# Kernel optimization log

Measured on AMD Instinct MI355X. Metric: run time of the kernel, lower is better.

Reference implementation:

```python
import jax, jax.numpy as jnp
import numpy as np
import itertools

L, F, T = 16, 2, 2**19          # levels, features/level, hashmap size
BASE, SCALE = 16, 1.5           # base resolution, per-level scale
N = 524288                      # batch of sample points
PRIMES = np.array([1, 2654435761, 805459861, 3674653429], dtype=np.uint32)


def hash_encode(x, table):
    """Multi-resolution hash-grid encoding. x: [N,d] in [0,1); table: [L,T,F]."""
    n, d = x.shape
    corners = jnp.asarray(list(itertools.product([0, 1], repeat=d)), dtype=jnp.uint32)  # [C,d]
    primes = jnp.asarray(PRIMES[:d])
    is_hi = corners.astype(bool)[None]          # [1,C,d]
    outs = []
    for l in range(L):
        res = float(np.floor(BASE * SCALE**l))
        pos = x * res
        p0f = jnp.floor(pos)
        frac = pos - p0f                         # [N,d]
        p0 = p0f.astype(jnp.uint32)
        coords = p0[:, None, :] + corners[None]  # [N,C,d] uint32 (wraps)
        m = coords * primes                      # [N,C,d]
        h = m[..., 0]
        for j in range(1, d):
            h = h ^ m[..., j]
        idx = (h % np.uint32(T)).astype(jnp.int32)              # [N,C]
        w = jnp.where(is_hi, frac[:, None, :], 1.0 - frac[:, None, :]).prod(-1)  # [N,C]
        feat = table[l][idx]                                    # [N,C,F]
        outs.append(jnp.einsum('nc,ncf->nf', w, feat))
    return jnp.concatenate(outs, axis=-1)        # [N, L*F]


def mlp(h, w_in, w_hid, w_out):
    """tcnn-style bias-free MLP, ReLU hidden, linear output."""
    h = jax.nn.relu(h @ w_in)
    for i in range(w_hid.shape[0]):
        h = jax.nn.relu(h @ w_hid[i])
    return h @ w_out


def setup_inputs() -> dict:
    key = jax.random.key(0)
    ks = jax.random.split(key, 20)
    def w(k, shape):
        fan = shape[-2]
        return jax.random.normal(k, shape, jnp.float32) / np.sqrt(fan).astype(np.float32)
    return {
        'x': jax.random.uniform(ks[0], (N, 3), jnp.float32),
        't': jax.random.uniform(ks[1], (1,), jnp.float32),
        'skip_alpha': jax.random.uniform(ks[2], (1,), jnp.float32),
        'table_s': jax.random.normal(ks[3], (L, T, F), jnp.float32) * 1e-2,
        'ws_in': w(ks[4], (32, 64)),
        'ws_hid': w(ks[5], (3, 64, 64)),
        'ws_out': w(ks[6], (64, 64)),
        'table_d': jax.random.normal(ks[7], (L, T, F), jnp.float32) * 1e-2,
        'wd_in': w(ks[8], (32, 64)),
        'wd_hid': w(ks[9], (3, 64, 64)),
        'wd_out': w(ks[10], (64, 64)),
        'w1_in': w(ks[11], (128, 64)),
        'w1_hid': w(ks[12], (1, 64, 64)),
        'w1_out': w(ks[13], (64, 128)),
        'w2_in': w(ks[14], (128, 64)),
        'w2_hid': w(ks[15], (1, 64, 64)),
        'w2_out': w(ks[16], (64, 1)),
    }


def reference(x, t, skip_alpha, table_s, ws_in, ws_hid, ws_out,
              table_d, wd_in, wd_hid, wd_out,
              w1_in, w1_hid, w1_out, w2_in, w2_hid, w2_out):
    static_features = mlp(hash_encode(x, table_s), ws_in, ws_hid, ws_out)          # [N,64]
    t_col = jnp.broadcast_to(t, (x.shape[0], 1))
    x4 = jnp.concatenate([x, t_col], axis=1)                                        # [N,4]
    dynamic_features = mlp(hash_encode(x4, table_d), wd_in, wd_hid, wd_out)        # [N,64]
    features = jnp.concatenate([static_features, dynamic_features], axis=-1)       # [N,128]
    out1 = mlp(features, w1_in, w1_hid, w1_out)                                     # [N,128]
    blended = out1 * skip_alpha + (1.0 - skip_alpha) * features
    return mlp(blended, w2_in, w2_hid, w2_out)                                      # [N,1]
```

## Files before the change

kernel.cpp:

```cpp
#include <hip/hip_runtime.h>
#include <hip/hip_bf16.h>
#include <stdint.h>

#define LVLS 16
#define TSZ  524288
#define TMASK 0x7FFFFu
#define NPTS 524288
#define P1 2654435761u
#define P2 805459861u
#define P3 3674653429u

__constant__ float RES_TAB[16] = {
    16.f, 24.f, 36.f, 54.f, 81.f, 121.f, 182.f, 273.f,
    410.f, 615.f, 922.f, 1383.f, 2075.f, 3113.f, 4670.f, 7006.f};

using f16x8 = __attribute__((ext_vector_type(8))) _Float16;
using f32x4 = __attribute__((ext_vector_type(4))) float;
using u32x8 = __attribute__((ext_vector_type(8))) uint32_t;

union PackF16 { uint32_t u; _Float16 h[2]; };

constexpr int PS = 72;

struct WPtrs { const float* p[11]; };

__global__ void k_build(const float* __restrict__ ts, const float* __restrict__ td,
                        const float* __restrict__ tptr, uint2* __restrict__ Tc,
                        WPtrs wp, _Float16* __restrict__ wdst) {
    int B = blockIdx.x;
    int tid = threadIdx.x;
    if (B < 40960) {
        int c = B & 7, j = B >> 3;
        int l, i;
        if (j < 1024) {
            l = c >> 1;
            i = (c & 1) * 262144 + j * 256 + tid;
        } else if (j < 3072) {
            l = 12 + (c >> 1);
            i = (j - 1024) * 256 + tid;
        } else {
            l = 4 + c;
            i = (j - 3072) * 256 + tid;
        }
        int id = l * TSZ + i;
        float2 sv = ((const float2*)ts)[id];
        float res = RES_TAB[l];
        float tv  = tptr[0];
        float pt  = tv * res;
        float fpt = floorf(pt);
        float ft  = pt - fpt;
        uint32_t ut = (uint32_t)(int)fpt;
        uint32_t h0 = (ut * P3) & TMASK;
        uint32_t h1 = ((ut + 1u) * P3) & TMASK;
        const float2* tdl = (const float2*)td + (size_t)l * TSZ;
        float2 a = tdl[i ^ h0];
        float2 b = tdl[i ^ h1];
        PackF16 o0, o1;
        o0.h[0] = (_Float16)sv.x; o0.h[1] = (_Float16)sv.y;
        o1.h[0] = (_Float16)((1.f - ft) * a.x + ft * b.x);
        o1.h[1] = (_Float16)((1.f - ft) * a.y + ft * b.y);
        Tc[id] = make_uint2(o0.u, o1.u);
    } else {
        int id = (B - 40960) * 256 + tid;
        if (id >= 69632) return;
        const int OFF[16] = {0,2048,6144,10240,14336,18432,20480,24576,28672,
                             32768,36864,45056,49152,57344,65536,69632};
        const int KK[15]  = {32,64,64,64,64,32,64,64,64,64,128,64,64,128,64};
        const int NN[15]  = {64,64,64,64,64,64,64,64,64,64,64,64,128,64,64};
        const int PSEL[15]= {0,1,1,1,2,3,4,4,4,5,6,7,8,9,10};
        const int POFF[15]= {0,0,4096,8192,0,0,0,4096,8192,0,0,0,0,0,0};
        int m = 0;
        while (id >= OFF[m+1]) m++;
        int local = id - OFF[m];
        int jj   = local & 7;
        int lane = (local >> 3) & 63;
        int blk  = local >> 9;
        int KC   = KK[m] >> 5;
        int ct   = blk / KC;
        int kc   = blk - ct * KC;
        int k    = kc*32 + ((lane>>4)<<3) + jj;
        int n    = ct*16 + (lane & 15);
        const float* src = wp.p[PSEL[m]] + POFF[m];
        wdst[id] = (_Float16)src[k * NN[m] + n];
    }
}

template<int Q>
__device__ __forceinline__ void enc_batch(const float* __restrict__ x,
                                          const uint2* __restrict__ tcl, float res,
                                          uint32_t* __restrict__ es,
                                          uint32_t* __restrict__ ed,
                                          int p0, int stride) {
    static_assert(Q == 4, "pin fence written for Q=4");
    u32x8 v8[Q*2];
    float wx[Q], wy[Q], wz[Q];
#pragma unroll
    for (int q = 0; q < Q; q++) {
        int p = p0 + q * stride;
        float px = x[p*3+0]*res, py = x[p*3+1]*res, pz = x[p*3+2]*res;
        float fx = floorf(px), fy = floorf(py), fz = floorf(pz);
        wx[q] = px-fx; wy[q] = py-fy; wz[q] = pz-fz;
        uint32_t ux = (uint32_t)(int)fx, uy = (uint32_t)(int)fy, uz = (uint32_t)(int)fz;
        uint32_t hx[2] = {ux, ux + 1u};
        uint32_t hy[2] = {uy * P1, (uy + 1u) * P1};
        uint32_t hz[2] = {uz * P2, (uz + 1u) * P2};
#pragma unroll
        for (int c = 0; c < 8; c++) {
            uint32_t idx = (hx[c&1] ^ hy[(c>>1)&1] ^ hz[c>>2]) & TMASK;
            uint2 t = tcl[idx];
            v8[q*2 + (c>>2)][(c&3)*2 + 0] = t.x;
            v8[q*2 + (c>>2)][(c&3)*2 + 1] = t.y;
        }
    }
    asm volatile("" : "+v"(v8[0]), "+v"(v8[1]), "+v"(v8[2]), "+v"(v8[3]),
                      "+v"(v8[4]), "+v"(v8[5]), "+v"(v8[6]), "+v"(v8[7]));
#pragma unroll
    for (int q = 0; q < Q; q++) {
        float wxa[2] = {1.f-wx[q], wx[q]};
        float wya[2] = {1.f-wy[q], wy[q]};
        float wza[2] = {1.f-wz[q], wz[q]};
        float sA0 = 0.f, sA1 = 0.f, sD0 = 0.f, sD1 = 0.f;
#pragma unroll
        for (int c = 0; c < 8; c++) {
            float w = wxa[c&1] * wya[(c>>1)&1] * wza[c>>2];
            PackF16 s, d;
            s.u = v8[q*2 + (c>>2)][(c&3)*2 + 0];
            d.u = v8[q*2 + (c>>2)][(c&3)*2 + 1];
            sA0 += w * (float)s.h[0]; sA1 += w * (float)s.h[1];
            sD0 += w * (float)d.h[0]; sD1 += w * (float)d.h[1];
        }
        int p = p0 + q * stride;
        PackF16 o;
        o.h[0] = (_Float16)sA0; o.h[1] = (_Float16)sA1; es[p] = o.u;
        o.h[0] = (_Float16)sD0; o.h[1] = (_Float16)sD1; ed[p] = o.u;
    }
}

__launch_bounds__(256, 4)
__global__ void k_encode(const float* __restrict__ x,
                         const uint2* __restrict__ Tc,
                         uint32_t* __restrict__ EncS, uint32_t* __restrict__ EncD) {
    int tid = threadIdx.x;
    int c   = blockIdx.x & 7;
    int b   = blockIdx.x >> 3;
    int l, pb, stride;
    if (b < 512) {
        l = 4 + c;
        pb = b * 256 + tid;
        stride = 131072;
    } else if (b < 768) {
        l = 12 + (c >> 1);
        pb = (c & 1) * 262144 + (b - 512) * 256 + tid;
        stride = 65536;
    } else {
        l = c >> 1;
        pb = (c & 1) * 262144 + (b - 768) * 256 + tid;
        stride = 65536;
    }
    const uint2* tcl = Tc + (size_t)l * TSZ;
    uint32_t* es = EncS + (size_t)l * NPTS;
    uint32_t* ed = EncD + (size_t)l * NPTS;
    float res = RES_TAB[l];
    enc_batch<4>(x, tcl, res, es, ed, pb, stride);
}

__device__ __forceinline__ void wait_lds() {
    asm volatile("s_waitcnt lgkmcnt(0)" ::: "memory");
}

template<int KC, bool RELU>
__device__ __forceinline__ void mm2(const f16x8 a[2][4], const f16x8* __restrict__ B,
                                    _Float16* dst, int m, int quad, int lane) {
#pragma unroll
    for (int ct = 0; ct < 4; ct++) {
        f32x4 acc0 = {0.f,0.f,0.f,0.f}, acc1 = {0.f,0.f,0.f,0.f};
#pragma unroll
        for (int kc = 0; kc < KC; kc++) {
            f16x8 b = B[(ct*KC+kc)*64 + lane];
            acc0 = __builtin_amdgcn_mfma_f32_16x16x32_f16(a[0][kc], b, acc0, 0, 0, 0);
            acc1 = __builtin_amdgcn_mfma_f32_16x16x32_f16(a[1][kc], b, acc1, 0, 0, 0);
        }
#pragma unroll
        for (int i = 0; i < 4; i++) {
            float v0 = acc0[i], v1 = acc1[i];
            if (RELU) { v0 = fmaxf(v0, 0.f); v1 = fmaxf(v1, 0.f); }
            dst[(0*16 + quad*4+i)*PS + ct*16 + m] = (_Float16)v0;
            dst[(1*16 + quad*4+i)*PS + ct*16 + m] = (_Float16)v1;
        }
    }
}

template<int KC>
__device__ __forceinline__ void mm2_keep(const f16x8 a[2][4], const f16x8* __restrict__ B,
                                         _Float16* dst, PackF16 P[2][8],
                                         int m, int quad, int lane) {
#pragma unroll
    for (int ct = 0; ct < 4; ct++) {
        f32x4 acc0 = {0.f,0.f,0.f,0.f}, acc1 = {0.f,0.f,0.f,0.f};
#pragma unroll
        for (int kc = 0; kc < KC; kc++) {
            f16x8 b = B[(ct*KC+kc)*64 + lane];
            acc0 = __builtin_amdgcn_mfma_f32_16x16x32_f16(a[0][kc], b, acc0, 0, 0, 0);
            acc1 = __builtin_amdgcn_mfma_f32_16x16x32_f16(a[1][kc], b, acc1, 0, 0, 0);
        }
#pragma unroll
        for (int ih = 0; ih < 2; ih++) {
            PackF16 p0, p1;
            p0.h[0] = (_Float16)acc0[ih*2+0]; p0.h[1] = (_Float16)acc0[ih*2+1];
            p1.h[0] = (_Float16)acc1[ih*2+0]; p1.h[1] = (_Float16)acc1[ih*2+1];
            P[0][ct*2+ih] = p0; P[1][ct*2+ih] = p1;
            dst[(0*16 + quad*4+ih*2+0)*PS + ct*16 + m] = p0.h[0];
            dst[(0*16 + quad*4+ih*2+1)*PS + ct*16 + m] = p0.h[1];
            dst[(1*16 + quad*4+ih*2+0)*PS + ct*16 + m] = p1.h[0];
            dst[(1*16 + quad*4+ih*2+1)*PS + ct*16 + m] = p1.h[1];
        }
    }
}

template<int KC>
__device__ __forceinline__ void read_a(const _Float16* buf, f16x8 a[2][4], int m, int quad) {
#pragma unroll
    for (int rt = 0; rt < 2; rt++)
#pragma unroll
        for (int kc = 0; kc < KC; kc++)
            a[rt][kc] = *(const f16x8*)(buf + (rt*16 + m)*PS + kc*32 + quad*8);
}

__device__ __forceinline__ void read_a128(const _Float16* Fs, const _Float16* Fd,
                                          f16x8 a[2][4], int m, int quad) {
#pragma unroll
    for (int rt = 0; rt < 2; rt++) {
#pragma unroll
        for (int kc = 0; kc < 2; kc++) {
            a[rt][kc]   = *(const f16x8*)(Fs + (rt*16 + m)*PS + kc*32 + quad*8);
            a[rt][kc+2] = *(const f16x8*)(Fd + (rt*16 + m)*PS + kc*32 + quad*8);
        }
    }
}

__device__ __forceinline__ void load_enc(const uint32_t* __restrict__ Enc,
                                         int pbase, int m, int quad, f16x8 a[2][4]) {
#pragma unroll
    for (int rt = 0; rt < 2; rt++) {
        union { uint32_t u[4]; f16x8 v; } cv;
        int p = pbase + rt*16 + m;
#pragma unroll
        for (int j = 0; j < 4; j++)
            cv.u[j] = Enc[(size_t)(quad*4 + j) * NPTS + p];
        a[rt][0] = cv.v;
    }
}

__launch_bounds__(256, 4)
__global__ void k_mlp(const uint32_t* __restrict__ EncS, const uint32_t* __restrict__ EncD,
                      const _Float16* __restrict__ Wfrag, const float* __restrict__ alphap,
                      const float* __restrict__ w2out, float* __restrict__ out) {
    __shared__ _Float16 FsB[4][32*PS];
    __shared__ _Float16 FdB[4][32*PS];
    int tid  = threadIdx.x;
    int wave = tid >> 6, lane = tid & 63;
    int m = lane & 15, quad = lane >> 4;
    int pbase = blockIdx.x * 128 + wave * 32;
    _Float16* Fs = FsB[wave];
    _Float16* Fd = FdB[wave];
    const f16x8* W8 = (const f16x8*)Wfrag;
    float alpha = alphap[0];

    f16x8 a[2][4];
    PackF16 sP[2][8], dP[2][8];

    load_enc(EncS, pbase, m, quad, a);
    mm2<1, true>(a, W8 + 0,    Fs, m, quad, lane); wait_lds();
    read_a<2>(Fs, a, m, quad);
    mm2<2, true>(a, W8 + 256,  Fs, m, quad, lane); wait_lds();
    read_a<2>(Fs, a, m, quad);
    mm2<2, true>(a, W8 + 768,  Fs, m, quad, lane); wait_lds();
    read_a<2>(Fs, a, m, quad);
    mm2<2, true>(a, W8 + 1280, Fs, m, quad, lane); wait_lds();
    read_a<2>(Fs, a, m, quad);
    mm2_keep<2>(a, W8 + 1792, Fs, sP, m, quad, lane);
    load_enc(EncD, pbase, m, quad, a);
    mm2<1, true>(a, W8 + 2304, Fd, m, quad, lane); wait_lds();
    read_a<2>(Fd, a, m, quad);
    mm2<2, true>(a, W8 + 2560, Fd, m, quad, lane); wait_lds();
    read_a<2>(Fd, a, m, quad);
    mm2<2, true>(a, W8 + 3072, Fd, m, quad, lane); wait_lds();
    read_a<2>(Fd, a, m, quad);
    mm2<2, true>(a, W8 + 3584, Fd, m, quad, lane); wait_lds();
    read_a<2>(Fd, a, m, quad);
    mm2_keep<2>(a, W8 + 4096, Fd, dP, m, quad, lane); wait_lds();
    read_a128(Fs, Fd, a, m, quad);
    mm2<4, true>(a, W8 + 4608, Fs, m, quad, lane); wait_lds();
    read_a<2>(Fs, a, m, quad);
    mm2<2, true>(a, W8 + 5632, Fs, m, quad, lane); wait_lds();
    read_a<2>(Fs, a, m, quad);
#pragma unroll
    for (int ct = 0; ct < 8; ct++) {
        f32x4 acc0 = {0.f,0.f,0.f,0.f}, acc1 = {0.f,0.f,0.f,0.f};
#pragma unroll
        for (int kc = 0; kc < 2; kc++) {
            f16x8 b = W8[6144 + (ct*2+kc)*64 + lane];
            acc0 = __builtin_amdgcn_mfma_f32_16x16x32_f16(a[0][kc], b, acc0, 0, 0, 0);
            acc1 = __builtin_amdgcn_mfma_f32_16x16x32_f16(a[1][kc], b, acc1, 0, 0, 0);
        }
        _Float16* tgt = (ct < 4) ? Fs : Fd;
        int col = (ct & 3) * 16 + m;
#pragma unroll
        for (int i = 0; i < 4; i++) {
            float f0 = (ct < 4) ? (float)sP[0][ct*2 + (i>>1)].h[i&1]
                                : (float)dP[0][(ct-4)*2 + (i>>1)].h[i&1];
            float f1 = (ct < 4) ? (float)sP[1][ct*2 + (i>>1)].h[i&1]
                                : (float)dP[1][(ct-4)*2 + (i>>1)].h[i&1];
            tgt[(0*16 + quad*4+i)*PS + col] = (_Float16)(alpha*acc0[i] + (1.f-alpha)*f0);
            tgt[(1*16 + quad*4+i)*PS + col] = (_Float16)(alpha*acc1[i] + (1.f-alpha)*f1);
        }
    }
    wait_lds();
    read_a128(Fs, Fd, a, m, quad);
    mm2<4, true>(a, W8 + 7168, Fs, m, quad, lane); wait_lds();
    read_a<2>(Fs, a, m, quad);
    float rsum0[4] = {0.f,0.f,0.f,0.f}, rsum1[4] = {0.f,0.f,0.f,0.f};
#pragma unroll
    for (int ct = 0; ct < 4; ct++) {
        f32x4 acc0 = {0.f,0.f,0.f,0.f}, acc1 = {0.f,0.f,0.f,0.f};
#pragma unroll
        for (int kc = 0; kc < 2; kc++) {
            f16x8 b = W8[8192 + (ct*2+kc)*64 + lane];
            acc0 = __builtin_amdgcn_mfma_f32_16x16x32_f16(a[0][kc], b, acc0, 0, 0, 0);
            acc1 = __builtin_amdgcn_mfma_f32_16x16x32_f16(a[1][kc], b, acc1, 0, 0, 0);
        }
        float wv = w2out[ct*16 + m];
#pragma unroll
        for (int i = 0; i < 4; i++) {
            rsum0[i] += fmaxf(acc0[i], 0.f) * wv;
            rsum1[i] += fmaxf(acc1[i], 0.f) * wv;
        }
    }
#pragma unroll
    for (int off = 1; off < 16; off <<= 1) {
#pragma unroll
        for (int i = 0; i < 4; i++) {
            rsum0[i] += __shfl_xor(rsum0[i], off, 64);
            rsum1[i] += __shfl_xor(rsum1[i], off, 64);
        }
    }
    if (m == 0) {
#pragma unroll
        for (int i = 0; i < 4; i++) {
            out[pbase + 0*16 + quad*4 + i] = rsum0[i];
            out[pbase + 1*16 + quad*4 + i] = rsum1[i];
        }
    }
}

extern "C" void kernel_launch(void* const* d_in, const int* in_sizes, int n_in,
                              void* d_out, int out_size, void* d_ws, size_t ws_size,
                              hipStream_t stream) {
    const float* x      = (const float*)d_in[0];
    const float* t      = (const float*)d_in[1];
    const float* alpha  = (const float*)d_in[2];
    const float* tab_s  = (const float*)d_in[3];
    const float* ws_in  = (const float*)d_in[4];
    const float* ws_hid = (const float*)d_in[5];
    const float* ws_out = (const float*)d_in[6];
    const float* tab_d  = (const float*)d_in[7];
    const float* wd_in  = (const float*)d_in[8];
    const float* wd_hid = (const float*)d_in[9];
    const float* wd_out = (const float*)d_in[10];
    const float* w1_in  = (const float*)d_in[11];
    const float* w1_hid = (const float*)d_in[12];
    const float* w1_out = (const float*)d_in[13];
    const float* w2_in  = (const float*)d_in[14];
    const float* w2_hid = (const float*)d_in[15];
    const float* w2_out = (const float*)d_in[16];
    float* out = (float*)d_out;

    char* ws = (char*)d_ws;
    _Float16* Wfrag = (_Float16*)ws;
    uint2*    Tc    = (uint2*)(ws + 139264);
    uint32_t* EncS  = (uint32_t*)(ws + 139264 + 67108864);
    uint32_t* EncD  = EncS + (size_t)LVLS * NPTS;
    size_t needed = 139264 + 67108864 + 2ull * 33554432ull;
    if (ws_size < needed) return;

    WPtrs wp;
    wp.p[0] = ws_in;  wp.p[1] = ws_hid; wp.p[2] = ws_out;
    wp.p[3] = wd_in;  wp.p[4] = wd_hid; wp.p[5] = wd_out;
    wp.p[6] = w1_in;  wp.p[7] = w1_hid; wp.p[8] = w1_out;
    wp.p[9] = w2_in;  wp.p[10] = w2_hid;

    k_build  <<<41232, 256, 0, stream>>>(tab_s, tab_d, t, Tc, wp, Wfrag);
    k_encode <<<8192,  256, 0, stream>>>(x, Tc, EncS, EncD);
    k_mlp    <<<NPTS/128, 256, 0, stream>>>(EncS, EncD, Wfrag, alpha, w2_out, out);
}
```

Measured before the change: 590.8 us.

## Software-pipeline hash-grid gathers with double-buffered point batches in encode kernel

The encode kernel now handles 8 points per thread instead of 4 and launches half as many blocks. Table gathers are split into two register buffers, so loads for the next pair of points are in flight while the previous pair is interpolated and stored. Empty asm pins and memory fences keep the compiler from reordering the stages. The aim is to hide gather latency inside each thread, at the cost of higher register pressure and fewer waves in the grid.

```diff
diff --git a/kernel.cpp b/kernel.cpp
--- a/kernel.cpp
+++ b/kernel.cpp
@@ -85,56 +85,47 @@
     }
 }
 
-template<int Q>
-__device__ __forceinline__ void enc_batch(const float* __restrict__ x,
-                                          const uint2* __restrict__ tcl, float res,
-                                          uint32_t* __restrict__ es,
-                                          uint32_t* __restrict__ ed,
-                                          int p0, int stride) {
-    static_assert(Q == 4, "pin fence written for Q=4");
-    u32x8 v8[Q*2];
-    float wx[Q], wy[Q], wz[Q];
-#pragma unroll
-    for (int q = 0; q < Q; q++) {
-        int p = p0 + q * stride;
-        float px = x[p*3+0]*res, py = x[p*3+1]*res, pz = x[p*3+2]*res;
-        float fx = floorf(px), fy = floorf(py), fz = floorf(pz);
-        wx[q] = px-fx; wy[q] = py-fy; wz[q] = pz-fz;
-        uint32_t ux = (uint32_t)(int)fx, uy = (uint32_t)(int)fy, uz = (uint32_t)(int)fz;
-        uint32_t hx[2] = {ux, ux + 1u};
-        uint32_t hy[2] = {uy * P1, (uy + 1u) * P1};
-        uint32_t hz[2] = {uz * P2, (uz + 1u) * P2};
-#pragma unroll
-        for (int c = 0; c < 8; c++) {
-            uint32_t idx = (hx[c&1] ^ hy[(c>>1)&1] ^ hz[c>>2]) & TMASK;
-            uint2 t = tcl[idx];
-            v8[q*2 + (c>>2)][(c&3)*2 + 0] = t.x;
-            v8[q*2 + (c>>2)][(c&3)*2 + 1] = t.y;
-        }
-    }
-    asm volatile("" : "+v"(v8[0]), "+v"(v8[1]), "+v"(v8[2]), "+v"(v8[3]),
-                      "+v"(v8[4]), "+v"(v8[5]), "+v"(v8[6]), "+v"(v8[7]));
-#pragma unroll
-    for (int q = 0; q < Q; q++) {
-        float wxa[2] = {1.f-wx[q], wx[q]};
-        float wya[2] = {1.f-wy[q], wy[q]};
-        float wza[2] = {1.f-wz[q], wz[q]};
-        float sA0 = 0.f, sA1 = 0.f, sD0 = 0.f, sD1 = 0.f;
-#pragma unroll
-        for (int c = 0; c < 8; c++) {
-            float w = wxa[c&1] * wya[(c>>1)&1] * wza[c>>2];
-            PackF16 s, d;
-            s.u = v8[q*2 + (c>>2)][(c&3)*2 + 0];
-            d.u = v8[q*2 + (c>>2)][(c&3)*2 + 1];
-            sA0 += w * (float)s.h[0]; sA1 += w * (float)s.h[1];
-            sD0 += w * (float)d.h[0]; sD1 += w * (float)d.h[1];
-        }
-        int p = p0 + q * stride;
-        PackF16 o;
-        o.h[0] = (_Float16)sA0; o.h[1] = (_Float16)sA1; es[p] = o.u;
-        o.h[0] = (_Float16)sD0; o.h[1] = (_Float16)sD1; ed[p] = o.u;
-    }
-}
+__device__ __forceinline__ void gather1(const uint2* __restrict__ tcl,
+                                        float px, float py, float pz,
+                                        u32x8& va, u32x8& vb,
+                                        float& wx, float& wy, float& wz) {
+    float fx = floorf(px), fy = floorf(py), fz = floorf(pz);
+    wx = px - fx; wy = py - fy; wz = pz - fz;
+    uint32_t ux = (uint32_t)(int)fx, uy = (uint32_t)(int)fy, uz = (uint32_t)(int)fz;
+    uint32_t hx0 = ux,     hx1 = ux + 1u;
+    uint32_t hy0 = uy*P1,  hy1 = (uy+1u)*P1;
+    uint32_t hz0 = uz*P2,  hz1 = (uz+1u)*P2;
+#pragma unroll
+    for (int cc = 0; cc < 8; cc++) {
+        uint32_t idx = (((cc&1)?hx1:hx0) ^ ((cc&2)?hy1:hy0) ^ ((cc&4)?hz1:hz0)) & TMASK;
+        uint2 t = tcl[idx];
+        if (cc < 4) { va[(cc&3)*2+0] = t.x; va[(cc&3)*2+1] = t.y; }
+        else        { vb[(cc&3)*2+0] = t.x; vb[(cc&3)*2+1] = t.y; }
+    }
+}
+
+__device__ __forceinline__ void consume1(const u32x8& va, const u32x8& vb,
+                                         float wx, float wy, float wz,
+                                         uint32_t* __restrict__ es,
+                                         uint32_t* __restrict__ ed, int p) {
+    float wxa[2] = {1.f-wx, wx}, wya[2] = {1.f-wy, wy}, wza[2] = {1.f-wz, wz};
+    float sA0 = 0.f, sA1 = 0.f, sD0 = 0.f, sD1 = 0.f;
+#pragma unroll
+    for (int cc = 0; cc < 8; cc++) {
+        float w = wxa[cc&1] * wya[(cc>>1)&1] * wza[cc>>2];
+        PackF16 s, d;
+        s.u = (cc<4) ? va[(cc&3)*2+0] : vb[(cc&3)*2+0];
+        d.u = (cc<4) ? va[(cc&3)*2+1] : vb[(cc&3)*2+1];
+        sA0 += w*(float)s.h[0]; sA1 += w*(float)s.h[1];
+        sD0 += w*(float)d.h[0]; sD1 += w*(float)d.h[1];
+    }
+    PackF16 o;
+    o.h[0] = (_Float16)sA0; o.h[1] = (_Float16)sA1; es[p] = o.u;
+    o.h[0] = (_Float16)sD0; o.h[1] = (_Float16)sD1; ed[p] = o.u;
+}
+
+#define MEMFENCE asm volatile("" ::: "memory")
+#define PIN(a,b,c,d) asm volatile("" : "+v"(a), "+v"(b), "+v"(c), "+v"(d))
 
 __launch_bounds__(256, 4)
 __global__ void k_encode(const float* __restrict__ x,
@@ -144,24 +135,58 @@
     int c   = blockIdx.x & 7;
     int b   = blockIdx.x >> 3;
     int l, pb, stride;
-    if (b < 512) {
+    if (b < 256) {
         l = 4 + c;
         pb = b * 256 + tid;
-        stride = 131072;
-    } else if (b < 768) {
+        stride = 65536;
+    } else if (b < 384) {
         l = 12 + (c >> 1);
-        pb = (c & 1) * 262144 + (b - 512) * 256 + tid;
-        stride = 65536;
+        pb = (c & 1) * 262144 + (b - 256) * 256 + tid;
+        stride = 32768;
     } else {
         l = c >> 1;
-        pb = (c & 1) * 262144 + (b - 768) * 256 + tid;
-        stride = 65536;
+        pb = (c & 1) * 262144 + (b - 384) * 256 + tid;
+        stride = 32768;
     }
     const uint2* tcl = Tc + (size_t)l * TSZ;
     uint32_t* es = EncS + (size_t)l * NPTS;
     uint32_t* ed = EncD + (size_t)l * NPTS;
     float res = RES_TAB[l];
-    enc_batch<4>(x, tcl, res, es, ed, pb, stride);
+
+    float PX[8], PY[8], PZ[8];
+#pragma unroll
+    for (int i = 0; i < 8; i++) {
+        int p = pb + i * stride;
+        PX[i] = x[p*3+0]*res; PY[i] = x[p*3+1]*res; PZ[i] = x[p*3+2]*res;
+    }
+
+    u32x8 A0, A1, A2, A3, B0, B1, B2, B3;
+    float wA0x, wA0y, wA0z, wA1x, wA1y, wA1z;
+    float wB0x, wB0y, wB0z, wB1x, wB1y, wB1z;
+
+    gather1(tcl, PX[0], PY[0], PZ[0], A0, A1, wA0x, wA0y, wA0z);
+    gather1(tcl, PX[1], PY[1], PZ[1], A2, A3, wA1x, wA1y, wA1z);
+    gather1(tcl, PX[2], PY[2], PZ[2], B0, B1, wB0x, wB0y, wB0z);
+    gather1(tcl, PX[3], PY[3], PZ[3], B2, B3, wB1x, wB1y, wB1z);
+    MEMFENCE;
+    PIN(A0, A1, A2, A3);
+    consume1(A0, A1, wA0x, wA0y, wA0z, es, ed, pb + 0*stride);
+    consume1(A2, A3, wA1x, wA1y, wA1z, es, ed, pb + 1*stride);
+    gather1(tcl, PX[4], PY[4], PZ[4], A0, A1, wA0x, wA0y, wA0z);
+    gather1(tcl, PX[5], PY[5], PZ[5], A2, A3, wA1x, wA1y, wA1z);
+    MEMFENCE;
+    PIN(B0, B1, B2, B3);
+    consume1(B0, B1, wB0x, wB0y, wB0z, es, ed, pb + 2*stride);
+    consume1(B2, B3, wB1x, wB1y, wB1z, es, ed, pb + 3*stride);
+    gather1(tcl, PX[6], PY[6], PZ[6], B0, B1, wB0x, wB0y, wB0z);
+    gather1(tcl, PX[7], PY[7], PZ[7], B2, B3, wB1x, wB1y, wB1z);
+    MEMFENCE;
+    PIN(A0, A1, A2, A3);
+    consume1(A0, A1, wA0x, wA0y, wA0z, es, ed, pb + 4*stride);
+    consume1(A2, A3, wA1x, wA1y, wA1z, es, ed, pb + 5*stride);
+    PIN(B0, B1, B2, B3);
+    consume1(B0, B1, wB0x, wB0y, wB0z, es, ed, pb + 6*stride);
+    consume1(B2, B3, wB1x, wB1y, wB1z, es, ed, pb + 7*stride);
 }
 
 __device__ __forceinline__ void wait_lds() {
@@ -390,6 +415,6 @@
     wp.p[9] = w2_in;  wp.p[10] = w2_hid;
 
     k_build  <<<41232, 256, 0, stream>>>(tab_s, tab_d, t, Tc, wp, Wfrag);
-    k_encode <<<8192,  256, 0, stream>>>(x, Tc, EncS, EncD);
+    k_encode <<<4096,  256, 0, stream>>>(x, Tc, EncS, EncD);
     k_mlp    <<<NPTS/128, 256, 0, stream>>>(EncS, EncD, Wfrag, alpha, w2_out, out);
 }
```

New measurement: 545.9 us. -7.6%, faster.
